# Performance work log

Measured on AMD Instinct MI355X. Metric: run time of the kernel, lower is better.

Reference implementation:

```python
import jax, jax.numpy as jnp
import numpy as np

EMB_DIM = 1024
N_HEADS = 16
HEAD_DIM = EMB_DIM // N_HEADS


def setup_inputs() -> dict:
    key = jax.random.key(0)
    ks = jax.random.split(key, 6)
    B, S, D = 2, 2048, EMB_DIM
    scale = 1.0 / np.sqrt(D)
    return {
        "in_data": jax.random.normal(ks[0], (B, S, D), dtype=jnp.float32),
        "Wq": jax.random.normal(ks[1], (D, D), dtype=jnp.float32) * scale,
        "Wk": jax.random.normal(ks[2], (D, D), dtype=jnp.float32) * scale,
        "Wv": jax.random.normal(ks[3], (D, D), dtype=jnp.float32) * scale,
        "Wo": jax.random.normal(ks[4], (D, D), dtype=jnp.float32) * scale,
        "bo": jax.random.normal(ks[5], (D,), dtype=jnp.float32) * 0.01,
    }


def reference(in_data, Wq, Wk, Wv, Wo, bo):
    B, S, D = in_data.shape
    H, Hd = N_HEADS, HEAD_DIM
    # Linear projections (qvbias=False): torch Linear is x @ W.T
    q = in_data @ Wq.T
    k = in_data @ Wk.T
    v = in_data @ Wv.T
    # split heads -> (B, H, S, Hd)
    q = q.reshape(B, S, H, Hd).transpose(0, 2, 1, 3)
    k = k.reshape(B, S, H, Hd).transpose(0, 2, 1, 3)
    v = v.reshape(B, S, H, Hd).transpose(0, 2, 1, 3)
    # scores (B, H, S, S), causal mask applied BEFORE scaling (as in source)
    scores = jnp.einsum("bhqd,bhkd->bhqk", q, k)
    causal = jnp.triu(jnp.ones((S, S), dtype=bool), k=1)
    scores = jnp.where(causal, -jnp.inf, scores)
    scores = scores / jnp.sqrt(jnp.asarray(Hd, dtype=scores.dtype))
    attn = jax.nn.softmax(scores, axis=-1)
    # dropout with drop_rate=0.0 -> identity
    ctx = jnp.einsum("bhqk,bhkd->bhqd", attn, v)
    ctx = ctx.transpose(0, 2, 1, 3).reshape(B, S, D)
    out = ctx @ Wo.T + bo
    return out
```

## Files before the change

### kernel.cpp

```cpp
#include <hip/hip_runtime.h>

typedef _Float16 f16;
typedef _Float16 f16x2 __attribute__((ext_vector_type(2)));
typedef _Float16 f16x4 __attribute__((ext_vector_type(4)));
typedef _Float16 f16x8 __attribute__((ext_vector_type(8)));
typedef float f32x4 __attribute__((ext_vector_type(4)));
typedef int i32x4 __attribute__((ext_vector_type(4)));

#define MFMA(a, b, c) __builtin_amdgcn_mfma_f32_16x16x32_f16((a), (b), (c), 0, 0, 0)

typedef __attribute__((address_space(1))) const void gvoid;
typedef __attribute__((address_space(3))) void lvoid;

__device__ __forceinline__ void gload16(const void* g, void* l) {
    __builtin_amdgcn_global_load_lds((gvoid*)g, (lvoid*)l, 16, 0, 0);
}

__global__ void cast_all(const float* __restrict__ x,
                         const float* __restrict__ w0, const float* __restrict__ w1,
                         const float* __restrict__ w2, const float* __restrict__ w3,
                         f16* __restrict__ xb, f16* __restrict__ wb) {
    const int NX = 4096 * 1024;
    int i = (blockIdx.x * 256 + threadIdx.x) * 4;
    if (i < NX) {
        float4 v = *(const float4*)(x + i);
        f16x4 o = {(f16)v.x, (f16)v.y, (f16)v.z, (f16)v.w};
        *(f16x4*)(xb + i) = o;
    } else {
        int j = i - NX;
        const float* s = (j < (1 << 20)) ? w0 : (j < (2 << 20)) ? w1
                       : (j < (3 << 20)) ? w2 : w3;
        int loc = j & ((1 << 20) - 1);
        float4 v = *(const float4*)(s + loc);
        f16x4 o = {(f16)v.x, (f16)v.y, (f16)v.z, (f16)v.w};
        *(f16x4*)(wb + j) = o;
    }
}

__global__ __launch_bounds__(256) void gemm_qkv(const f16* __restrict__ A,
                                                const f16* __restrict__ W,
                                                f16* __restrict__ Qo,
                                                f16* __restrict__ Ko,
                                                f16* __restrict__ VTo) {
    __shared__ __align__(16) f16 A0[128 * 64];
    __shared__ __align__(16) f16 A1[128 * 64];
    __shared__ __align__(16) f16 B0[3][64 * 64];
    __shared__ __align__(16) f16 B1[3][64 * 64];
    const int tid = threadIdx.x;
    const int lane = tid & 63, w = tid >> 6;
    const int lo = lane & 15, hi = lane >> 4;
    const int wr = w >> 1, wc = w & 1;
    const int m0 = blockIdx.x * 128, n0 = blockIdx.y * 64;
    const char* Ab = (const char*)A;
    const char* Wb = (const char*)W;

    f32x4 acc[3][4][2];
#pragma unroll
    for (int z = 0; z < 3; ++z)
#pragma unroll
        for (int i = 0; i < 4; ++i)
#pragma unroll
            for (int j = 0; j < 2; ++j) acc[z][i][j] = (f32x4){0.f, 0.f, 0.f, 0.f};

    auto stage = [&](f16* Ad, f16 (*Bd)[64 * 64], int kt) {
        const int kb = kt * 128;
#pragma unroll
        for (int rr = 0; rr < 4; ++rr) {
            int o = rr * 4096 + tid * 16;
            int row = o >> 7;
            int colB = (o & 127) ^ ((row & 7) << 4);
            gload16(Ab + (size_t)(m0 + row) * 2048 + kb + colB, (char*)Ad + o);
        }
#pragma unroll
        for (int z = 0; z < 3; ++z)
#pragma unroll
            for (int rr = 0; rr < 2; ++rr) {
                int o = rr * 4096 + tid * 16;
                int row = o >> 7;
                int colB = (o & 127) ^ ((row & 7) << 4);
                gload16(Wb + (size_t)z * 2097152 + (size_t)(n0 + row) * 2048 + kb + colB,
                        (char*)&Bd[z][0] + o);
            }
    };

    auto compute = [&](const f16* Al, const f16 (*Bl)[64 * 64]) {
#pragma unroll
        for (int kc = 0; kc < 2; ++kc) {
            f16x8 af[4];
#pragma unroll
            for (int f = 0; f < 4; ++f) {
                const int row = wr * 64 + f * 16 + lo;
                const int cb = (kc * 64 + hi * 16) ^ ((row & 7) << 4);
                af[f] = *(const f16x8*)((const char*)Al + row * 128 + cb);
            }
#pragma unroll
            for (int z = 0; z < 3; ++z) {
                f16x8 bf[2];
#pragma unroll
                for (int f = 0; f < 2; ++f) {
                    const int row = wc * 32 + f * 16 + lo;
                    const int cb = (kc * 64 + hi * 16) ^ ((row & 7) << 4);
                    bf[f] = *(const f16x8*)((const char*)&Bl[z][0] + row * 128 + cb);
                }
#pragma unroll
                for (int i = 0; i < 4; ++i)
#pragma unroll
                    for (int j = 0; j < 2; ++j)
                        acc[z][i][j] = MFMA(af[i], bf[j], acc[z][i][j]);
            }
        }
    };

    stage(&A0[0], B0, 0);
    for (int kt = 0; kt < 16; ++kt) {
        __syncthreads();
        if ((kt & 1) == 0) {
            if (kt < 15) stage(&A1[0], B1, kt + 1);
            compute(&A0[0], B0);
        } else {
            if (kt < 15) stage(&A0[0], B0, kt + 1);
            compute(&A1[0], B1);
        }
    }

    const int mb = m0 + wr * 64 + hi * 4;
    const int nb = n0 + wc * 32 + lo;
#pragma unroll
    for (int i = 0; i < 4; ++i)
#pragma unroll
        for (int j = 0; j < 2; ++j)
#pragma unroll
            for (int r = 0; r < 4; ++r) {
                const int m = mb + i * 16 + r, n = nb + j * 16;
                Qo[(size_t)m * 1024 + n] = (f16)(acc[0][i][j][r] * 0.18033688f);
                Ko[(size_t)m * 1024 + n] = (f16)acc[1][i][j][r];
                VTo[(size_t)((m >> 11) * 1024 + n) * 2048 + (m & 2047)] =
                    (f16)acc[2][i][j][r];
            }
}

__global__ __launch_bounds__(256) void attn(const f16* __restrict__ Q,
                                            const f16* __restrict__ K,
                                            const f16* __restrict__ VT,
                                            f16* __restrict__ CTX) {
    __shared__ __align__(16) f16 K0[64 * 64];
    __shared__ __align__(16) f16 K1[64 * 64];
    __shared__ __align__(16) f16 V0[64 * 64];
    __shared__ __align__(16) f16 V1[64 * 64];
    const int tid = threadIdx.x;
    const int lane = tid & 63, w = tid >> 6;
    const int lo = lane & 15, hi = lane >> 4;
    const int bh = blockIdx.x;
    const int qt = 31 - blockIdx.y;
    const int b = bh >> 4, h = bh & 15;
    const int qw0 = qt * 64 + w * 16;
    const int qglob = qw0 + lo;

    const f16* qrow = Q + (size_t)(b * 2048 + qw0 + lo) * 1024 + h * 64 + hi * 8;
    const f16x8 qa0 = *(const f16x8*)(qrow);
    const f16x8 qa1 = *(const f16x8*)(qrow + 32);

    f32x4 ctx[4];
#pragma unroll
    for (int d = 0; d < 4; ++d) ctx[d] = (f32x4){0.f, 0.f, 0.f, 0.f};
    float mrun = -3e38f, lsum = 0.f;

    const int idx0 = (2 * (hi & 1)) * 16 + lo;
    const int idx1 = idx0 + 16;

    const char* Kb = (const char*)K;
    const char* Vb = (const char*)VT;

    auto stage = [&](f16* Kd, f16* Vd, int t) {
        const int kv0 = t * 64;
#pragma unroll
        for (int rr = 0; rr < 2; ++rr) {
            int o = rr * 4096 + tid * 16;
            int row = o >> 7;
            int colB = (o & 127) ^ ((row & 7) << 4);
            gload16(Kb + (size_t)(b * 2048 + kv0 + row) * 2048 + h * 128 + colB,
                    (char*)Kd + o);
            gload16(Vb + (size_t)(b * 1024 + h * 64 + row) * 4096 + (size_t)kv0 * 2 + colB,
                    (char*)Vd + o);
        }
    };

    auto compute = [&](const f16* Klb, const f16* Vlb, int t) {
        f32x4 s4[4];
        __builtin_amdgcn_s_setprio(1);
#pragma unroll
        for (int fj = 0; fj < 4; ++fj) {
            f32x4 a = (f32x4){0.f, 0.f, 0.f, 0.f};
            const int kv = fj * 16 + lo;
#pragma unroll
            for (int kc = 0; kc < 2; ++kc) {
                const int cb = (kc * 64 + hi * 16) ^ ((kv & 7) << 4);
                f16x8 kf = *(const f16x8*)((const char*)Klb + kv * 128 + cb);
                a = MFMA(kf, kc ? qa1 : qa0, a);
            }
            s4[fj] = a;
        }
        __builtin_amdgcn_s_setprio(0);

        float pv[16];
        if (t == qt) {
#pragma unroll
            for (int fj = 0; fj < 4; ++fj)
#pragma unroll
                for (int r = 0; r < 4; ++r) {
                    const int kvg = t * 64 + fj * 16 + hi * 4 + r;
                    pv[fj * 4 + r] = (kvg > qglob) ? -1e38f : s4[fj][r];
                }
        } else {
#pragma unroll
            for (int fj = 0; fj < 4; ++fj)
#pragma unroll
                for (int r = 0; r < 4; ++r) pv[fj * 4 + r] = s4[fj][r];
        }

        float tm[8];
#pragma unroll
        for (int i = 0; i < 8; ++i) tm[i] = fmaxf(pv[i], pv[i + 8]);
#pragma unroll
        for (int i = 0; i < 4; ++i) tm[i] = fmaxf(tm[i], tm[i + 4]);
        const float mxl = fmaxf(fmaxf(tm[0], tm[1]), fmaxf(tm[2], tm[3]));

        if (__any(mxl > mrun + 8.0f)) {
            float mxg = fmaxf(mxl, __shfl_xor(mxl, 16));
            mxg = fmaxf(mxg, __shfl_xor(mxg, 32));
            const float mnew = fmaxf(mrun, mxg);
            const float corr = __builtin_amdgcn_exp2f(mrun - mnew);
            mrun = mnew;
            lsum *= corr;
#pragma unroll
            for (int d = 0; d < 4; ++d) {
                ctx[d][0] *= corr; ctx[d][1] *= corr;
                ctx[d][2] *= corr; ctx[d][3] *= corr;
            }
        }

#pragma unroll
        for (int i = 0; i < 16; ++i) pv[i] = __builtin_amdgcn_exp2f(pv[i] - mrun);
        float ts[8];
#pragma unroll
        for (int i = 0; i < 8; ++i) ts[i] = pv[i] + pv[i + 8];
#pragma unroll
        for (int i = 0; i < 4; ++i) ts[i] = ts[i] + ts[i + 4];
        lsum += (ts[0] + ts[1]) + (ts[2] + ts[3]);

        int ph[4][2];
#pragma unroll
        for (int fj = 0; fj < 4; ++fj)
#pragma unroll
            for (int r2 = 0; r2 < 2; ++r2) {
                f16x2 hpair = {(f16)pv[fj * 4 + 2 * r2], (f16)pv[fj * 4 + 2 * r2 + 1]};
                ph[fj][r2] = __builtin_bit_cast(int, hpair);
            }

        f16x8 pb[2];
#pragma unroll
        for (int kc = 0; kc < 2; ++kc) {
            i32x4 dw;
#pragma unroll
            for (int j2 = 0; j2 < 4; ++j2) {
                const int idx = (j2 < 2) ? idx0 : idx1;
                int vA = __shfl(ph[2 * kc][j2 & 1], idx);
                int vB = __shfl(ph[2 * kc + 1][j2 & 1], idx);
                dw[j2] = (hi & 2) ? vB : vA;
            }
            pb[kc] = __builtin_bit_cast(f16x8, dw);
        }

        __builtin_amdgcn_s_setprio(1);
#pragma unroll
        for (int df = 0; df < 4; ++df) {
            const int d = df * 16 + lo;
#pragma unroll
            for (int kc = 0; kc < 2; ++kc) {
                const int cb = (kc * 64 + hi * 16) ^ ((d & 7) << 4);
                f16x8 vf = *(const f16x8*)((const char*)Vlb + d * 128 + cb);
                ctx[df] = MFMA(vf, pb[kc], ctx[df]);
            }
        }
        __builtin_amdgcn_s_setprio(0);
    };

    stage(&K0[0], &V0[0], 0);
    for (int t = 0; t <= qt; ++t) {
        __syncthreads();
        if ((t & 1) == 0) {
            if (t < qt) stage(&K1[0], &V1[0], t + 1);
            compute(&K0[0], &V0[0], t);
        } else {
            if (t < qt) stage(&K0[0], &V0[0], t + 1);
            compute(&K1[0], &V1[0], t);
        }
    }

    float lt = lsum + __shfl_xor(lsum, 16);
    lt += __shfl_xor(lt, 32);
    const float inv = 1.0f / lt;
#pragma unroll
    for (int df = 0; df < 4; ++df) {
        f16x4 o = {(f16)(ctx[df][0] * inv), (f16)(ctx[df][1] * inv),
                   (f16)(ctx[df][2] * inv), (f16)(ctx[df][3] * inv)};
        *(f16x4*)(CTX + (size_t)(b * 2048 + qw0 + lo) * 1024 + h * 64 + df * 16 + hi * 4) = o;
    }
}

__global__ __launch_bounds__(256) void gemm_proj(const f16* __restrict__ A,
                                                 const f16* __restrict__ Bw,
                                                 float* __restrict__ Co,
                                                 const float* __restrict__ bias) {
    __shared__ __align__(16) f16 A0[64 * 64];
    __shared__ __align__(16) f16 A1[64 * 64];
    __shared__ __align__(16) f16 B0[128 * 64];
    __shared__ __align__(16) f16 B1[128 * 64];
    const int tid = threadIdx.x;
    const int lane = tid & 63, w = tid >> 6;
    const int lo = lane & 15, hi = lane >> 4;
    const int m0 = blockIdx.x * 64, n0 = blockIdx.y * 128;
    const char* Ab = (const char*)A;
    const char* Bb = (const char*)Bw;

    f32x4 acc[4][2];
#pragma unroll
    for (int i = 0; i < 4; ++i) {
        acc[i][0] = (f32x4){0.f, 0.f, 0.f, 0.f};
        acc[i][1] = (f32x4){0.f, 0.f, 0.f, 0.f};
    }

    auto stage = [&](f16* Ad, f16* Bd, int kt) {
        const int kb = kt * 128;
#pragma unroll
        for (int rr = 0; rr < 2; ++rr) {
            int o = rr * 4096 + tid * 16;
            int row = o >> 7;
            int colB = (o & 127) ^ ((row & 7) << 4);
            gload16(Ab + (size_t)(m0 + row) * 2048 + kb + colB, (char*)Ad + o);
        }
#pragma unroll
        for (int rr = 0; rr < 4; ++rr) {
            int o = rr * 4096 + tid * 16;
            int row = o >> 7;
            int colB = (o & 127) ^ ((row & 7) << 4);
            gload16(Bb + (size_t)(n0 + row) * 2048 + kb + colB, (char*)Bd + o);
        }
    };

    auto compute = [&](const f16* Al, const f16* Bl) {
#pragma unroll
        for (int kc = 0; kc < 2; ++kc) {
            f16x8 af[4], bf[2];
#pragma unroll
            for (int f = 0; f < 4; ++f) {
                const int row = f * 16 + lo;
                const int cb = (kc * 64 + hi * 16) ^ ((row & 7) << 4);
                af[f] = *(const f16x8*)((const char*)Al + row * 128 + cb);
            }
#pragma unroll
            for (int f = 0; f < 2; ++f) {
                const int row = w * 32 + f * 16 + lo;
                const int cb = (kc * 64 + hi * 16) ^ ((row & 7) << 4);
                bf[f] = *(const f16x8*)((const char*)Bl + row * 128 + cb);
            }
#pragma unroll
            for (int i = 0; i < 4; ++i)
#pragma unroll
                for (int j = 0; j < 2; ++j) acc[i][j] = MFMA(af[i], bf[j], acc[i][j]);
        }
    };

    stage(&A0[0], &B0[0], 0);
    for (int kt = 0; kt < 16; ++kt) {
        __syncthreads();
        if ((kt & 1) == 0) {
            if (kt < 15) stage(&A1[0], &B1[0], kt + 1);
            compute(&A0[0], &B0[0]);
        } else {
            if (kt < 15) stage(&A0[0], &B0[0], kt + 1);
            compute(&A1[0], &B1[0]);
        }
    }

    const int mbase = m0 + hi * 4;
    const int nbase = n0 + w * 32 + lo;
#pragma unroll
    for (int j = 0; j < 2; ++j) {
        float bj = bias[nbase + j * 16];
#pragma unroll
        for (int i = 0; i < 4; ++i)
#pragma unroll
            for (int r = 0; r < 4; ++r)
                Co[(size_t)(mbase + i * 16 + r) * 1024 + nbase + j * 16] =
                    acc[i][j][r] + bj;
    }
}

extern "C" void kernel_launch(void* const* d_in, const int* in_sizes, int n_in,
                              void* d_out, int out_size, void* d_ws, size_t ws_size,
                              hipStream_t stream) {
    const float* x = (const float*)d_in[0];
    const float* wq = (const float*)d_in[1];
    const float* wk = (const float*)d_in[2];
    const float* wv = (const float*)d_in[3];
    const float* wo = (const float*)d_in[4];
    const float* bo = (const float*)d_in[5];

    const size_t M1 = 1024 * 1024;
    f16* VT = (f16*)d_ws;
    f16* Wh = VT + 4 * M1;
    f16* QKV = Wh + 4 * M1;
    f16* Xb = QKV + 8 * M1;
    f16* Q = QKV;
    f16* K = QKV + 4 * M1;
    f16* CTX = QKV + 8 * M1;
    float* out = (float*)d_out;

    cast_all<<<dim3(8192), dim3(256), 0, stream>>>(x, wq, wk, wv, wo, Xb, Wh);
    gemm_qkv<<<dim3(32, 16), dim3(256), 0, stream>>>(Xb, Wh, Q, K, VT);
    attn<<<dim3(32, 32), dim3(256), 0, stream>>>(Q, K, VT, CTX);
    gemm_proj<<<dim3(64, 8), dim3(256), 0, stream>>>(CTX, Wh + 3 * M1, out, bo);
}
```

Measured before the change: 185.8 us.

## Split QKV GEMM per projection, enlarge attention tiles, shrink proj tiles

```diff
diff --git a/kernel.cpp b/kernel.cpp
--- a/kernel.cpp
+++ b/kernel.cpp
@@ -42,104 +42,101 @@
                                                 f16* __restrict__ Qo,
                                                 f16* __restrict__ Ko,
                                                 f16* __restrict__ VTo) {
-    __shared__ __align__(16) f16 A0[128 * 64];
-    __shared__ __align__(16) f16 A1[128 * 64];
-    __shared__ __align__(16) f16 B0[3][64 * 64];
-    __shared__ __align__(16) f16 B1[3][64 * 64];
+    __shared__ __align__(16) f16 As[128 * 64];
+    __shared__ __align__(16) f16 Bs[64 * 64];
     const int tid = threadIdx.x;
     const int lane = tid & 63, w = tid >> 6;
     const int lo = lane & 15, hi = lane >> 4;
     const int wr = w >> 1, wc = w & 1;
-    const int m0 = blockIdx.x * 128, n0 = blockIdx.y * 64;
+    const int m0 = blockIdx.x * 128;
+    const int by = blockIdx.y;
+    const int z = by >> 4;
+    const int n0 = (by & 15) * 64;
     const char* Ab = (const char*)A;
-    const char* Wb = (const char*)W;
-
-    f32x4 acc[3][4][2];
-#pragma unroll
-    for (int z = 0; z < 3; ++z)
-#pragma unroll
-        for (int i = 0; i < 4; ++i)
-#pragma unroll
-            for (int j = 0; j < 2; ++j) acc[z][i][j] = (f32x4){0.f, 0.f, 0.f, 0.f};
-
-    auto stage = [&](f16* Ad, f16 (*Bd)[64 * 64], int kt) {
+    const char* Wb = (const char*)W + (size_t)z * 2097152;
+
+    f32x4 acc[4][2];
+#pragma unroll
+    for (int i = 0; i < 4; ++i) {
+        acc[i][0] = (f32x4){0.f, 0.f, 0.f, 0.f};
+        acc[i][1] = (f32x4){0.f, 0.f, 0.f, 0.f};
+    }
+
+    for (int kt = 0; kt < 16; ++kt) {
         const int kb = kt * 128;
 #pragma unroll
         for (int rr = 0; rr < 4; ++rr) {
             int o = rr * 4096 + tid * 16;
             int row = o >> 7;
             int colB = (o & 127) ^ ((row & 7) << 4);
-            gload16(Ab + (size_t)(m0 + row) * 2048 + kb + colB, (char*)Ad + o);
-        }
-#pragma unroll
-        for (int z = 0; z < 3; ++z)
-#pragma unroll
-            for (int rr = 0; rr < 2; ++rr) {
-                int o = rr * 4096 + tid * 16;
-                int row = o >> 7;
-                int colB = (o & 127) ^ ((row & 7) << 4);
-                gload16(Wb + (size_t)z * 2097152 + (size_t)(n0 + row) * 2048 + kb + colB,
-                        (char*)&Bd[z][0] + o);
-            }
-    };
-
-    auto compute = [&](const f16* Al, const f16 (*Bl)[64 * 64]) {
+            gload16(Ab + (size_t)(m0 + row) * 2048 + kb + colB, (char*)As + o);
+        }
+#pragma unroll
+        for (int rr = 0; rr < 2; ++rr) {
+            int o = rr * 4096 + tid * 16;
+            int row = o >> 7;
+            int colB = (o & 127) ^ ((row & 7) << 4);
+            gload16(Wb + (size_t)(n0 + row) * 2048 + kb + colB, (char*)Bs + o);
+        }
+        __syncthreads();
 #pragma unroll
         for (int kc = 0; kc < 2; ++kc) {
-            f16x8 af[4];
+            f16x8 af[4], bf[2];
 #pragma unroll
             for (int f = 0; f < 4; ++f) {
                 const int row = wr * 64 + f * 16 + lo;
                 const int cb = (kc * 64 + hi * 16) ^ ((row & 7) << 4);
-                af[f] = *(const f16x8*)((const char*)Al + row * 128 + cb);
-            }
-#pragma unroll
-            for (int z = 0; z < 3; ++z) {
-                f16x8 bf[2];
-#pragma unroll
-                for (int f = 0; f < 2; ++f) {
-                    const int row = wc * 32 + f * 16 + lo;
-                    const int cb = (kc * 64 + hi * 16) ^ ((row & 7) << 4);
-                    bf[f] = *(const f16x8*)((const char*)&Bl[z][0] + row * 128 + cb);
-                }
-#pragma unroll
-                for (int i = 0; i < 4; ++i)
-#pragma unroll
-                    for (int j = 0; j < 2; ++j)
-                        acc[z][i][j] = MFMA(af[i], bf[j], acc[z][i][j]);
-            }
-        }
-    };
-
-    stage(&A0[0], B0, 0);
-    for (int kt = 0; kt < 16; ++kt) {
+                af[f] = *(const f16x8*)((const char*)As + row * 128 + cb);
+            }
+#pragma unroll
+            for (int f = 0; f < 2; ++f) {
+                const int row = wc * 32 + f * 16 + lo;
+                const int cb = (kc * 64 + hi * 16) ^ ((row & 7) << 4);
+                bf[f] = *(const f16x8*)((const char*)Bs + row * 128 + cb);
+            }
+#pragma unroll
+            for (int i = 0; i < 4; ++i)
+#pragma unroll
+                for (int j = 0; j < 2; ++j) acc[i][j] = MFMA(af[i], bf[j], acc[i][j]);
+        }
         __syncthreads();
-        if ((kt & 1) == 0) {
-            if (kt < 15) stage(&A1[0], B1, kt + 1);
-            compute(&A0[0], B0);
-        } else {
-            if (kt < 15) stage(&A0[0], B0, kt + 1);
-            compute(&A1[0], B1);
-        }
     }
 
     const int mb = m0 + wr * 64 + hi * 4;
     const int nb = n0 + wc * 32 + lo;
-#pragma unroll
-    for (int i = 0; i < 4; ++i)
-#pragma unroll
-        for (int j = 0; j < 2; ++j)
-#pragma unroll
-            for (int r = 0; r < 4; ++r) {
-                const int m = mb + i * 16 + r, n = nb + j * 16;
-                Qo[(size_t)m * 1024 + n] = (f16)(acc[0][i][j][r] * 0.18033688f);
-                Ko[(size_t)m * 1024 + n] = (f16)acc[1][i][j][r];
-                VTo[(size_t)((m >> 11) * 1024 + n) * 2048 + (m & 2047)] =
-                    (f16)acc[2][i][j][r];
-            }
-}
-
-__global__ __launch_bounds__(256) void attn(const f16* __restrict__ Q,
+    if (z == 0) {
+#pragma unroll
+        for (int i = 0; i < 4; ++i)
+#pragma unroll
+            for (int j = 0; j < 2; ++j)
+#pragma unroll
+                for (int r = 0; r < 4; ++r)
+                    Qo[(size_t)(mb + i * 16 + r) * 1024 + nb + j * 16] =
+                        (f16)(acc[i][j][r] * 0.18033688f);
+    } else if (z == 1) {
+#pragma unroll
+        for (int i = 0; i < 4; ++i)
+#pragma unroll
+            for (int j = 0; j < 2; ++j)
+#pragma unroll
+                for (int r = 0; r < 4; ++r)
+                    Ko[(size_t)(mb + i * 16 + r) * 1024 + nb + j * 16] =
+                        (f16)acc[i][j][r];
+    } else {
+#pragma unroll
+        for (int i = 0; i < 4; ++i)
+#pragma unroll
+            for (int j = 0; j < 2; ++j)
+#pragma unroll
+                for (int r = 0; r < 4; ++r) {
+                    const int m = mb + i * 16 + r, n = nb + j * 16;
+                    VTo[(size_t)((m >> 11) * 1024 + n) * 2048 + (m & 2047)] =
+                        (f16)acc[i][j][r];
+                }
+    }
+}
+
+__global__ __launch_bounds__(512) void attn(const f16* __restrict__ Q,
                                             const f16* __restrict__ K,
                                             const f16* __restrict__ VT,
                                             f16* __restrict__ CTX) {
@@ -151,10 +148,13 @@
     const int lane = tid & 63, w = tid >> 6;
     const int lo = lane & 15, hi = lane >> 4;
     const int bh = blockIdx.x;
-    const int qt = 31 - blockIdx.y;
+    const int qi = blockIdx.y;
+    const int qt = (qi < 8) ? qi : 23 - qi;
     const int b = bh >> 4, h = bh & 15;
-    const int qw0 = qt * 64 + w * 16;
+    const int qw0 = qt * 128 + w * 16;
     const int qglob = qw0 + lo;
+    const int ntb = qt * 2 + 2;
+    const int nt_w = qt * 2 + 1 + (w >> 2);
 
     const f16* qrow = Q + (size_t)(b * 2048 + qw0 + lo) * 1024 + h * 64 + hi * 8;
     const f16x8 qa0 = *(const f16x8*)(qrow);
@@ -173,19 +173,16 @@
 
     auto stage = [&](f16* Kd, f16* Vd, int t) {
         const int kv0 = t * 64;
-#pragma unroll
-        for (int rr = 0; rr < 2; ++rr) {
-            int o = rr * 4096 + tid * 16;
-            int row = o >> 7;
-            int colB = (o & 127) ^ ((row & 7) << 4);
-            gload16(Kb + (size_t)(b * 2048 + kv0 + row) * 2048 + h * 128 + colB,
-                    (char*)Kd + o);
-            gload16(Vb + (size_t)(b * 1024 + h * 64 + row) * 4096 + (size_t)kv0 * 2 + colB,
-                    (char*)Vd + o);
-        }
+        int o = tid * 16;
+        int row = o >> 7;
+        int colB = (o & 127) ^ ((row & 7) << 4);
+        gload16(Kb + (size_t)(b * 2048 + kv0 + row) * 2048 + h * 128 + colB,
+                (char*)Kd + o);
+        gload16(Vb + (size_t)(b * 1024 + h * 64 + row) * 4096 + (size_t)kv0 * 2 + colB,
+                (char*)Vd + o);
     };
 
-    auto compute = [&](const f16* Klb, const f16* Vlb, int t) {
+    auto compute = [&](const f16* Klb, const f16* Vlb, bool diag, int t) {
         f32x4 s4[4];
         __builtin_amdgcn_s_setprio(1);
 #pragma unroll
@@ -203,7 +200,7 @@
         __builtin_amdgcn_s_setprio(0);
 
         float pv[16];
-        if (t == qt) {
+        if (diag) {
 #pragma unroll
             for (int fj = 0; fj < 4; ++fj)
 #pragma unroll
@@ -286,14 +283,14 @@
     };
 
     stage(&K0[0], &V0[0], 0);
-    for (int t = 0; t <= qt; ++t) {
+    for (int t = 0; t < ntb; ++t) {
         __syncthreads();
         if ((t & 1) == 0) {
-            if (t < qt) stage(&K1[0], &V1[0], t + 1);
-            compute(&K0[0], &V0[0], t);
+            if (t + 1 < ntb) stage(&K1[0], &V1[0], t + 1);
+            if (t < nt_w) compute(&K0[0], &V0[0], t == nt_w - 1, t);
         } else {
-            if (t < qt) stage(&K0[0], &V0[0], t + 1);
-            compute(&K1[0], &V1[0], t);
+            if (t + 1 < ntb) stage(&K0[0], &V0[0], t + 1);
+            if (t < nt_w) compute(&K1[0], &V1[0], t == nt_w - 1, t);
         }
     }
 
@@ -312,87 +309,69 @@
                                                  const f16* __restrict__ Bw,
                                                  float* __restrict__ Co,
                                                  const float* __restrict__ bias) {
-    __shared__ __align__(16) f16 A0[64 * 64];
-    __shared__ __align__(16) f16 A1[64 * 64];
-    __shared__ __align__(16) f16 B0[128 * 64];
-    __shared__ __align__(16) f16 B1[128 * 64];
+    __shared__ __align__(16) f16 As[64 * 64];
+    __shared__ __align__(16) f16 Bs[64 * 64];
     const int tid = threadIdx.x;
     const int lane = tid & 63, w = tid >> 6;
     const int lo = lane & 15, hi = lane >> 4;
-    const int m0 = blockIdx.x * 64, n0 = blockIdx.y * 128;
+    const int wr = w >> 1, wc = w & 1;
+    const int m0 = blockIdx.x * 64, n0 = blockIdx.y * 64;
     const char* Ab = (const char*)A;
     const char* Bb = (const char*)Bw;
 
-    f32x4 acc[4][2];
-#pragma unroll
-    for (int i = 0; i < 4; ++i) {
-        acc[i][0] = (f32x4){0.f, 0.f, 0.f, 0.f};
-        acc[i][1] = (f32x4){0.f, 0.f, 0.f, 0.f};
-    }
-
-    auto stage = [&](f16* Ad, f16* Bd, int kt) {
+    f32x4 acc[2][2];
+    acc[0][0] = acc[0][1] = acc[1][0] = acc[1][1] = (f32x4){0.f, 0.f, 0.f, 0.f};
+
+    for (int kt = 0; kt < 16; ++kt) {
         const int kb = kt * 128;
 #pragma unroll
         for (int rr = 0; rr < 2; ++rr) {
             int o = rr * 4096 + tid * 16;
             int row = o >> 7;
             int colB = (o & 127) ^ ((row & 7) << 4);
-            gload16(Ab + (size_t)(m0 + row) * 2048 + kb + colB, (char*)Ad + o);
-        }
-#pragma unroll
-        for (int rr = 0; rr < 4; ++rr) {
+            gload16(Ab + (size_t)(m0 + row) * 2048 + kb + colB, (char*)As + o);
+        }
+#pragma unroll
+        for (int rr = 0; rr < 2; ++rr) {
             int o = rr * 4096 + tid * 16;
             int row = o >> 7;
             int colB = (o & 127) ^ ((row & 7) << 4);
-            gload16(Bb + (size_t)(n0 + row) * 2048 + kb + colB, (char*)Bd + o);
-        }
-    };
-
-    auto compute = [&](const f16* Al, const f16* Bl) {
+            gload16(Bb + (size_t)(n0 + row) * 2048 + kb + colB, (char*)Bs + o);
+        }
+        __syncthreads();
 #pragma unroll
         for (int kc = 0; kc < 2; ++kc) {
-            f16x8 af[4], bf[2];
-#pragma unroll
-            for (int f = 0; f < 4; ++f) {
-                const int row = f * 16 + lo;
+            f16x8 af[2], bf[2];
+#pragma unroll
+            for (int f = 0; f < 2; ++f) {
+                const int row = wr * 32 + f * 16 + lo;
                 const int cb = (kc * 64 + hi * 16) ^ ((row & 7) << 4);
-                af[f] = *(const f16x8*)((const char*)Al + row * 128 + cb);
+                af[f] = *(const f16x8*)((const char*)As + row * 128 + cb);
             }
 #pragma unroll
             for (int f = 0; f < 2; ++f) {
-                const int row = w * 32 + f * 16 + lo;
+                const int row = wc * 32 + f * 16 + lo;
                 const int cb = (kc * 64 + hi * 16) ^ ((row & 7) << 4);
-                bf[f] = *(const f16x8*)((const char*)Bl + row * 128 + cb);
-            }
-#pragma unroll
-            for (int i = 0; i < 4; ++i)
+                bf[f] = *(const f16x8*)((const char*)Bs + row * 128 + cb);
+            }
+#pragma unroll
+            for (int i = 0; i < 2; ++i)
 #pragma unroll
                 for (int j = 0; j < 2; ++j) acc[i][j] = MFMA(af[i], bf[j], acc[i][j]);
         }
-    };
-
-    stage(&A0[0], &B0[0], 0);
-    for (int kt = 0; kt < 16; ++kt) {
         __syncthreads();
-        if ((kt & 1) == 0) {
-            if (kt < 15) stage(&A1[0], &B1[0], kt + 1);
-            compute(&A0[0], &B0[0]);
-        } else {
-            if (kt < 15) stage(&A0[0], &B0[0], kt + 1);
-            compute(&A1[0], &B1[0]);
-        }
-    }
-
-    const int mbase = m0 + hi * 4;
-    const int nbase = n0 + w * 32 + lo;
+    }
+
+    const int mb = m0 + wr * 32 + hi * 4;
+    const int nb = n0 + wc * 32 + lo;
 #pragma unroll
     for (int j = 0; j < 2; ++j) {
-        float bj = bias[nbase + j * 16];
-#pragma unroll
-        for (int i = 0; i < 4; ++i)
+        float bj = bias[nb + j * 16];
+#pragma unroll
+        for (int i = 0; i < 2; ++i)
 #pragma unroll
             for (int r = 0; r < 4; ++r)
-                Co[(size_t)(mbase + i * 16 + r) * 1024 + nbase + j * 16] =
+                Co[(size_t)(mb + i * 16 + r) * 1024 + nb + j * 16] =
                     acc[i][j][r] + bj;
     }
 }
@@ -418,7 +397,7 @@
     float* out = (float*)d_out;
 
     cast_all<<<dim3(8192), dim3(256), 0, stream>>>(x, wq, wk, wv, wo, Xb, Wh);
-    gemm_qkv<<<dim3(32, 16), dim3(256), 0, stream>>>(Xb, Wh, Q, K, VT);
-    attn<<<dim3(32, 32), dim3(256), 0, stream>>>(Q, K, VT, CTX);
-    gemm_proj<<<dim3(64, 8), dim3(256), 0, stream>>>(CTX, Wh + 3 * M1, out, bo);
-}
+    gemm_qkv<<<dim3(32, 48), dim3(256), 0, stream>>>(Xb, Wh, Q, K, VT);
+    attn<<<dim3(32, 16), dim3(512), 0, stream>>>(Q, K, VT, CTX);
+    gemm_proj<<<dim3(64, 16), dim3(256), 0, stream>>>(CTX, Wh + 3 * M1, out, bo);
+}
```

New measurement: 183.7 us. No clear change (-1.1%).
